# Kernel tuning notes

Hardware: AMD Instinct MI355X
Metric: run time of the kernel (lower is better)

Reference implementation:

```python
import jax, jax.numpy as jnp
import numpy as np

D_MODEL = 1024
N_HEADS = 16
D_HEAD = D_MODEL // N_HEADS
WINDOW = 256
SCALE = D_HEAD ** -0.5


def setup_inputs() -> dict:
    key = jax.random.key(0)
    ks = jax.random.split(key, 5)
    B, S = 2, 2048
    x = jax.random.normal(ks[0], (B, S, D_MODEL), dtype=jnp.float32)
    # weights stored as [d_in, d_out] so forward is x @ W + b
    W_qkv = jax.random.normal(ks[1], (D_MODEL, 3 * D_MODEL), dtype=jnp.float32) * (D_MODEL ** -0.5)
    b_qkv = jnp.zeros((3 * D_MODEL,), dtype=jnp.float32)
    W_out = jax.random.normal(ks[2], (D_MODEL, D_MODEL), dtype=jnp.float32) * (D_MODEL ** -0.5)
    b_out = jnp.zeros((D_MODEL,), dtype=jnp.float32)
    return {"x": x, "W_qkv": W_qkv, "b_qkv": b_qkv, "W_out": W_out, "b_out": b_out}


def _window_mask(S):
    # Faithful to source: keep positions where (i <= j) & (i >= j - WINDOW + 1),
    # i = query index (rows), j = key index (cols). (Anti-causal window, as in repo.)
    idx = jnp.arange(S)
    keep = (idx[:, None] <= idx[None, :]) & (idx[:, None] >= idx[None, :] - WINDOW + 1)
    return keep  # [S, S] bool


def reference(x, W_qkv, b_qkv, W_out, b_out):
    B, S, D = x.shape
    qkv = x @ W_qkv + b_qkv                      # [B,S,3D]
    q, k, v = jnp.split(qkv, 3, axis=-1)
    def heads(t):
        return t.reshape(B, S, N_HEADS, D_HEAD).transpose(0, 2, 1, 3)  # [B,H,S,dh]
    q, k, v = heads(q), heads(k), heads(v)
    attn = jnp.einsum('bhid,bhjd->bhij', q, k) * SCALE  # [B,H,S,S]
    keep = _window_mask(S)
    attn = jnp.where(keep[None, None], attn, -jnp.inf)
    attn = jax.nn.softmax(attn, axis=-1)
    # dropout is identity in eval mode
    out = jnp.einsum('bhij,bhjd->bhid', attn, v)        # [B,H,S,dh]
    out = out.transpose(0, 2, 1, 3).reshape(B, S, D)
    return out @ W_out + b_out
```

## Files before the change

kernel.cpp:

```cpp
#include <hip/hip_runtime.h>

typedef __bf16 bf16x8 __attribute__((ext_vector_type(8)));
typedef float f32x4 __attribute__((ext_vector_type(4)));
typedef unsigned short u16x8 __attribute__((ext_vector_type(8)));
typedef unsigned short u16x4 __attribute__((ext_vector_type(4)));

#define MFMA16(a, b, c) __builtin_amdgcn_mfma_f32_16x16x32_bf16((a), (b), (c), 0, 0, 0)

#define WAIT_VM2  asm volatile("s_waitcnt vmcnt(2)" ::: "memory")
#define WAIT_VM0  asm volatile("s_waitcnt vmcnt(0)" ::: "memory")
#define WAIT_LGKM asm volatile("s_waitcnt lgkmcnt(0)" ::: "memory")
#define BAR       __builtin_amdgcn_s_barrier()

__device__ __forceinline__ unsigned short f2bf(float f) {
  union { float f; unsigned int i; } v; v.f = f;
  unsigned int u = v.i;
  u += 0x7fffu + ((u >> 16) & 1u);
  return (unsigned short)(u >> 16);
}

__device__ __forceinline__ void gload16(const void* g, void* l) {
  __builtin_amdgcn_global_load_lds(
      (const __attribute__((address_space(1))) unsigned int*)g,
      (__attribute__((address_space(3))) unsigned int*)l, 16, 0, 0);
}

__global__ __launch_bounds__(256) void convert_x(const float* __restrict__ X,
                                                 unsigned short* __restrict__ Xb) {
  size_t i = (size_t)(blockIdx.x * 256 + threadIdx.x) * 8;
  f32x4 f0 = *(const f32x4*)(X + i);
  f32x4 f1 = *(const f32x4*)(X + i + 4);
  u16x8 t;
#pragma unroll
  for (int j = 0; j < 4; ++j) { t[j] = f2bf(f0[j]); t[4 + j] = f2bf(f1[j]); }
  *(u16x8*)(Xb + i) = t;
}

__global__ __launch_bounds__(256) void transpose_w(const float* __restrict__ W,
                                                   unsigned short* __restrict__ Wt,
                                                   int N) {
  __shared__ unsigned short t[32][33];
  int tx = threadIdx.x & 31, ty = threadIdx.x >> 5;
  int bx = blockIdx.x;
  int by = blockIdx.y;
#pragma unroll
  for (int j = 0; j < 4; ++j) {
    int r = ty + j * 8;
    t[tx][r] = f2bf(W[(size_t)(by * 32 + r) * N + bx * 32 + tx]);
  }
  __syncthreads();
#pragma unroll
  for (int j = 0; j < 4; ++j) {
    int r = ty + j * 8;
    Wt[(size_t)(bx * 32 + r) * 1024 + by * 32 + tx] = t[r][tx];
  }
}

__global__ __launch_bounds__(512) void gemm_bt(
    const unsigned short* __restrict__ A, const unsigned short* __restrict__ Bt,
    const float* __restrict__ bias,
    unsigned short* __restrict__ O0, unsigned short* __restrict__ O1,
    unsigned short* __restrict__ O2, float* __restrict__ OF, int mode) {
  __shared__ __align__(16) unsigned short As0[128 * 32];
  __shared__ __align__(16) unsigned short Bs0[128 * 32];
  __shared__ __align__(16) unsigned short As1[128 * 32];
  __shared__ __align__(16) unsigned short Bs1[128 * 32];

  const int K = 1024;
  int tid = threadIdx.x;
  int lane = tid & 63, wave = tid >> 6, quad = lane >> 4, l16 = lane & 15;
  int wr = wave >> 2, wc = wave & 3;
  int m0 = blockIdx.x * 128, n0 = blockIdx.y * 128;

  int srow = tid >> 2, su = tid & 3;
  const unsigned short* ag = A + (size_t)(m0 + srow) * K + su * 8;
  const unsigned short* bg = Bt + (size_t)(n0 + srow) * K + su * 8;
  int loff = tid * 16;

  int abase = (wr * 64 + l16) * 64 + quad * 16;
  int bbase = (wc * 32 + l16) * 64 + quad * 16;

  f32x4 acc[4][2];
#pragma unroll
  for (int i = 0; i < 4; ++i)
#pragma unroll
    for (int j = 0; j < 2; ++j) acc[i][j] = f32x4{0.f, 0.f, 0.f, 0.f};

  auto STAGE = [&](int k0, char* Asb, char* Bsb) {
    gload16(ag + k0, Asb + loff);
    gload16(bg + k0, Bsb + loff);
  };
  auto COMPUTE = [&](const char* Asb, const char* Bsb) {
    bf16x8 af[4], bfr[2];
#pragma unroll
    for (int t = 0; t < 4; ++t)
      af[t] = *(const bf16x8*)(Asb + abase + t * 1024);
#pragma unroll
    for (int t = 0; t < 2; ++t)
      bfr[t] = *(const bf16x8*)(Bsb + bbase + t * 1024);
#pragma unroll
    for (int mt = 0; mt < 4; ++mt)
#pragma unroll
      for (int nt = 0; nt < 2; ++nt)
        acc[mt][nt] = MFMA16(af[mt], bfr[nt], acc[mt][nt]);
  };

  STAGE(0, (char*)As0, (char*)Bs0);
  for (int t = 0; t < 30; t += 2) {
    STAGE((t + 1) * 32, (char*)As1, (char*)Bs1);
    WAIT_VM2; BAR;
    COMPUTE((const char*)As0, (const char*)Bs0);
    WAIT_LGKM; BAR;
    STAGE((t + 2) * 32, (char*)As0, (char*)Bs0);
    WAIT_VM2; BAR;
    COMPUTE((const char*)As1, (const char*)Bs1);
    WAIT_LGKM; BAR;
  }
  STAGE(31 * 32, (char*)As1, (char*)Bs1);
  WAIT_VM2; BAR;
  COMPUTE((const char*)As0, (const char*)Bs0);
  WAIT_LGKM; BAR;
  WAIT_VM0; BAR;
  COMPUTE((const char*)As1, (const char*)Bs1);

  if (mode == 0) {
#pragma unroll
    for (int nt = 0; nt < 2; ++nt) {
      int n = n0 + wc * 32 + nt * 16 + l16;
      float bv = bias[n];
      int seg = n >> 10, cc = n & 1023, hh = cc >> 6, d = cc & 63;
#pragma unroll
      for (int mt = 0; mt < 4; ++mt) {
        int mb = m0 + wr * 64 + mt * 16 + quad * 4;
        int b = mb >> 11, s = mb & 2047;
        if (seg == 2) {
          u16x4 pk;
#pragma unroll
          for (int r = 0; r < 4; ++r) pk[r] = f2bf(acc[mt][nt][r] + bv);
          *(u16x4*)&O2[((size_t)((b << 4) + hh) * 64 + d) * 2048 + s] = pk;
        } else {
          unsigned short* O = seg ? O1 : O0;
#pragma unroll
          for (int r = 0; r < 4; ++r)
            O[((size_t)((b << 4) + hh) * 2048 + (s + r)) * 64 + d] = f2bf(acc[mt][nt][r] + bv);
        }
      }
    }
  } else {
#pragma unroll
    for (int nt = 0; nt < 2; ++nt) {
      int n = n0 + wc * 32 + nt * 16 + l16;
      float bv = bias[n];
#pragma unroll
      for (int mt = 0; mt < 4; ++mt) {
        int mb = m0 + wr * 64 + mt * 16 + quad * 4;
#pragma unroll
        for (int r = 0; r < 4; ++r)
          OF[(size_t)(mb + r) * 1024 + n] = acc[mt][nt][r] + bv;
      }
    }
  }
}

__global__ __launch_bounds__(256) void gemm_bt64(
    const unsigned short* __restrict__ A, const unsigned short* __restrict__ Bt,
    const float* __restrict__ bias, float* __restrict__ OF) {
  __shared__ __align__(16) unsigned short As0[64 * 32];
  __shared__ __align__(16) unsigned short Bs0[64 * 32];
  __shared__ __align__(16) unsigned short As1[64 * 32];
  __shared__ __align__(16) unsigned short Bs1[64 * 32];

  const int K = 1024;
  int tid = threadIdx.x;
  int lane = tid & 63, wave = tid >> 6, quad = lane >> 4, l16 = lane & 15;
  int wr = wave >> 1, wc = wave & 1;
  int m0 = blockIdx.x * 64, n0 = blockIdx.y * 64;

  int srow = tid >> 2, su = tid & 3;
  const unsigned short* ag = A + (size_t)(m0 + srow) * K + su * 8;
  const unsigned short* bg = Bt + (size_t)(n0 + srow) * K + su * 8;
  int loff = tid * 16;

  int abase = (wr * 32 + l16) * 64 + quad * 16;
  int bbase = (wc * 32 + l16) * 64 + quad * 16;

  f32x4 acc[2][2];
#pragma unroll
  for (int i = 0; i < 2; ++i)
#pragma unroll
    for (int j = 0; j < 2; ++j) acc[i][j] = f32x4{0.f, 0.f, 0.f, 0.f};

  auto STAGE = [&](int k0, char* Asb, char* Bsb) {
    gload16(ag + k0, Asb + loff);
    gload16(bg + k0, Bsb + loff);
  };
  auto COMPUTE = [&](const char* Asb, const char* Bsb) {
    bf16x8 af[2], bfr[2];
#pragma unroll
    for (int t = 0; t < 2; ++t) {
      af[t]  = *(const bf16x8*)(Asb + abase + t * 1024);
      bfr[t] = *(const bf16x8*)(Bsb + bbase + t * 1024);
    }
#pragma unroll
    for (int mt = 0; mt < 2; ++mt)
#pragma unroll
      for (int nt = 0; nt < 2; ++nt)
        acc[mt][nt] = MFMA16(af[mt], bfr[nt], acc[mt][nt]);
  };

  STAGE(0, (char*)As0, (char*)Bs0);
  for (int t = 0; t < 30; t += 2) {
    STAGE((t + 1) * 32, (char*)As1, (char*)Bs1);
    WAIT_VM2; BAR;
    COMPUTE((const char*)As0, (const char*)Bs0);
    WAIT_LGKM; BAR;
    STAGE((t + 2) * 32, (char*)As0, (char*)Bs0);
    WAIT_VM2; BAR;
    COMPUTE((const char*)As1, (const char*)Bs1);
    WAIT_LGKM; BAR;
  }
  STAGE(31 * 32, (char*)As1, (char*)Bs1);
  WAIT_VM2; BAR;
  COMPUTE((const char*)As0, (const char*)Bs0);
  WAIT_LGKM; BAR;
  WAIT_VM0; BAR;
  COMPUTE((const char*)As1, (const char*)Bs1);

#pragma unroll
  for (int nt = 0; nt < 2; ++nt) {
    int n = n0 + wc * 32 + nt * 16 + l16;
    float bv = bias[n];
#pragma unroll
    for (int mt = 0; mt < 2; ++mt) {
      int mb = m0 + wr * 32 + mt * 16 + quad * 4;
#pragma unroll
      for (int r = 0; r < 4; ++r)
        OF[(size_t)(mb + r) * 1024 + n] = acc[mt][nt][r] + bv;
    }
  }
}

__global__ __launch_bounds__(256) void attn_kernel(
    const unsigned short* __restrict__ Q, const unsigned short* __restrict__ Kq,
    const unsigned short* __restrict__ Vt, unsigned short* __restrict__ AO) {
  __shared__ __align__(16) unsigned short Ps[4][16][40];

  int bid = blockIdx.x;
  int qblk = bid & 31, h = (bid >> 5) & 15, b = bid >> 9;
  int q0 = qblk * 64;
  int tid = threadIdx.x, lane = tid & 63, wave = tid >> 6, quad = lane >> 4, l16 = lane & 15;

  const unsigned short* Qb = Q + (size_t)(((b << 4) + h) * 2048) * 64;
  const unsigned short* Kb = Kq + (size_t)(((b << 4) + h) * 2048) * 64;
  const unsigned short* Vb = Vt + (size_t)(((b << 4) + h) * 64) * 2048;

  int qg = q0 + wave * 16 + l16;
  bf16x8 qf0 = __builtin_bit_cast(bf16x8, *(const u16x8*)&Qb[(size_t)qg * 64 + quad * 8]);
  bf16x8 qf1 = __builtin_bit_cast(bf16x8, *(const u16x8*)&Qb[(size_t)qg * 64 + 32 + quad * 8]);

  float m = -1e30f, l = 0.f;
  f32x4 zero = {0.f, 0.f, 0.f, 0.f};
  f32x4 o[4];
#pragma unroll
  for (int i = 0; i < 4; ++i) o[i] = zero;

  const float SCALE = 0.125f;
  int pstart = (wave >= 2) ? 1 : 0;
  int pend = pstart + 8;

  for (int p = pstart; p <= pend; ++p) {
    int kbase = q0 + p * 32;

    f32x4 sc[2];
    __builtin_amdgcn_s_setprio(1);
#pragma unroll
    for (int t = 0; t < 2; ++t) {
      int krow = kbase + t * 16 + l16;
      krow = krow > 2047 ? 2047 : krow;
      bf16x8 kf0 = __builtin_bit_cast(bf16x8, *(const u16x8*)&Kb[(size_t)krow * 64 + quad * 8]);
      bf16x8 kf1 = __builtin_bit_cast(bf16x8, *(const u16x8*)&Kb[(size_t)krow * 64 + 32 + quad * 8]);
      f32x4 z = zero;
      z = MFMA16(kf0, qf0, z);
      z = MFMA16(kf1, qf1, z);
      sc[t] = z;
    }
    __builtin_amdgcn_s_setprio(0);

    bf16x8 vf[4];
    {
      int vcol = kbase + quad * 8;
      vcol = vcol > 2040 ? 2040 : vcol;
#pragma unroll
      for (int nt = 0; nt < 4; ++nt)
        vf[nt] = __builtin_bit_cast(bf16x8,
            *(const u16x8*)&Vb[(size_t)(nt * 16 + l16) * 2048 + vcol]);
    }

    float sv[2][4];
#pragma unroll
    for (int t = 0; t < 2; ++t)
#pragma unroll
      for (int r = 0; r < 4; ++r) {
        int kg = kbase + t * 16 + quad * 4 + r;
        bool valid = (kg >= qg) && (kg <= qg + 255) && (kg < 2048);
        sv[t][r] = valid ? sc[t][r] * SCALE : -1e30f;
      }

    float vmax = fmaxf(fmaxf(fmaxf(sv[0][0], sv[0][1]), fmaxf(sv[0][2], sv[0][3])),
                       fmaxf(fmaxf(sv[1][0], sv[1][1]), fmaxf(sv[1][2], sv[1][3])));
    vmax = fmaxf(vmax, __shfl_xor(vmax, 16));
    vmax = fmaxf(vmax, __shfl_xor(vmax, 32));
    float mnew = fmaxf(m, vmax);
    float alpha = __expf(m - mnew);
    m = mnew;
    float pe[2][4];
#pragma unroll
    for (int t = 0; t < 2; ++t)
#pragma unroll
      for (int r = 0; r < 4; ++r) {
        float e = __expf(sv[t][r] - mnew);
        pe[t][r] = (sv[t][r] > -5e29f) ? e : 0.f;
      }
    float rs = ((pe[0][0] + pe[0][1]) + (pe[0][2] + pe[0][3])) +
               ((pe[1][0] + pe[1][1]) + (pe[1][2] + pe[1][3]));
    rs += __shfl_xor(rs, 16);
    rs += __shfl_xor(rs, 32);
    l = l * alpha + rs;

    f32x4 av;
#pragma unroll
    for (int r = 0; r < 4; ++r) av[r] = __shfl(alpha, quad * 4 + r);
#pragma unroll
    for (int nt = 0; nt < 4; ++nt) o[nt] *= av;

#pragma unroll
    for (int t = 0; t < 2; ++t) {
      u16x4 pk;
#pragma unroll
      for (int r = 0; r < 4; ++r) pk[r] = f2bf(pe[t][r]);
      *(u16x4*)&Ps[wave][l16][t * 16 + quad * 4] = pk;
    }
    __threadfence_block();
    bf16x8 pf = __builtin_bit_cast(bf16x8, *(const u16x8*)&Ps[wave][l16][quad * 8]);

    __builtin_amdgcn_s_setprio(1);
#pragma unroll
    for (int nt = 0; nt < 4; ++nt)
      o[nt] = MFMA16(pf, vf[nt], o[nt]);
    __builtin_amdgcn_s_setprio(0);
  }

  __threadfence_block();
  float* Lf = (float*)&Ps[wave][0][0];
  Lf[l16] = l;
  __threadfence_block();
  float lr[4];
#pragma unroll
  for (int r = 0; r < 4; ++r) lr[r] = Lf[quad * 4 + r];

  unsigned short* dst = AO + ((size_t)(b * 2048 + q0 + wave * 16) * 1024) + h * 64;
#pragma unroll
  for (int nt = 0; nt < 4; ++nt)
#pragma unroll
    for (int r = 0; r < 4; ++r) {
      int qq = quad * 4 + r;
      dst[(size_t)qq * 1024 + nt * 16 + l16] = f2bf(o[nt][r] / lr[r]);
    }
}

extern "C" void kernel_launch(void* const* d_in, const int* in_sizes, int n_in,
                              void* d_out, int out_size, void* d_ws, size_t ws_size,
                              hipStream_t stream) {
  const float* x = (const float*)d_in[0];
  const float* W_qkv = (const float*)d_in[1];
  const float* b_qkv = (const float*)d_in[2];
  const float* W_out = (const float*)d_in[3];
  const float* b_out = (const float*)d_in[4];
  float* out = (float*)d_out;

  unsigned short* ws = (unsigned short*)d_ws;
  unsigned short* Qw  = ws;
  unsigned short* Kw  = ws + 4194304;
  unsigned short* Vw  = ws + 8388608;
  unsigned short* Wqt = ws + 12582912;
  unsigned short* AO  = ws + 12582912;
  unsigned short* Wot = ws;
  unsigned short* Xb  = (unsigned short*)d_out;

  dim3 blk(256);
  dim3 gblk(512);
  convert_x<<<dim3(2048), blk, 0, stream>>>(x, Xb);
  transpose_w<<<dim3(96, 32), blk, 0, stream>>>(W_qkv, Wqt, 3072);
  gemm_bt<<<dim3(32, 24), gblk, 0, stream>>>(Xb, Wqt, b_qkv, Qw, Kw, Vw, nullptr, 0);
  attn_kernel<<<dim3(1024), blk, 0, stream>>>(Qw, Kw, Vw, AO);
  transpose_w<<<dim3(32, 32), blk, 0, stream>>>(W_out, Wot, 1024);
  gemm_bt64<<<dim3(64, 16), blk, 0, stream>>>(AO, Wot, b_out, out);
}
```

Measured before the change: 175.7 us.

## Merge prep kernels, retile QKV GEMM, skip rescale when max unchanged

Combines the x conversion and both weight transposes into one prep launch and rearranges the workspace so V lives in the output buffer. The QKV GEMM moves from 512-thread 128x128 tiles to 256-thread 128x64 tiles, doubling the grid and adjusting the vmcnt waits. In attention, the output and normaliser rescale is done only when some lane's running max grows, which skips multiplies at the cost of a wave-wide vote and a branch. The aim is to cut launch overhead, raise occupancy and drop redundant softmax work.

After: 181.6 us. 1.03x slower.

```diff
diff --git a/kernel.cpp b/kernel.cpp
--- a/kernel.cpp
+++ b/kernel.cpp
@@ -7,6 +7,7 @@
 
 #define MFMA16(a, b, c) __builtin_amdgcn_mfma_f32_16x16x32_bf16((a), (b), (c), 0, 0, 0)
 
+#define WAIT_VM3  asm volatile("s_waitcnt vmcnt(3)" ::: "memory")
 #define WAIT_VM2  asm volatile("s_waitcnt vmcnt(2)" ::: "memory")
 #define WAIT_VM0  asm volatile("s_waitcnt vmcnt(0)" ::: "memory")
 #define WAIT_LGKM asm volatile("s_waitcnt lgkmcnt(0)" ::: "memory")
@@ -25,24 +26,26 @@
       (__attribute__((address_space(3))) unsigned int*)l, 16, 0, 0);
 }
 
-__global__ __launch_bounds__(256) void convert_x(const float* __restrict__ X,
-                                                 unsigned short* __restrict__ Xb) {
-  size_t i = (size_t)(blockIdx.x * 256 + threadIdx.x) * 8;
-  f32x4 f0 = *(const f32x4*)(X + i);
-  f32x4 f1 = *(const f32x4*)(X + i + 4);
-  u16x8 t;
-#pragma unroll
-  for (int j = 0; j < 4; ++j) { t[j] = f2bf(f0[j]); t[4 + j] = f2bf(f1[j]); }
-  *(u16x8*)(Xb + i) = t;
-}
-
-__global__ __launch_bounds__(256) void transpose_w(const float* __restrict__ W,
-                                                   unsigned short* __restrict__ Wt,
-                                                   int N) {
+__global__ __launch_bounds__(256) void prep(
+    const float* __restrict__ X, const float* __restrict__ Wq,
+    const float* __restrict__ Wo, unsigned short* __restrict__ Xb,
+    unsigned short* __restrict__ Wqt, unsigned short* __restrict__ Wot) {
   __shared__ unsigned short t[32][33];
+  int id = blockIdx.x;
+  if (id < 2048) {
+    size_t i = (size_t)(id * 256 + threadIdx.x) * 8;
+    f32x4 f0 = *(const f32x4*)(X + i);
+    f32x4 f1 = *(const f32x4*)(X + i + 4);
+    u16x8 tt;
+#pragma unroll
+    for (int j = 0; j < 4; ++j) { tt[j] = f2bf(f0[j]); tt[4 + j] = f2bf(f1[j]); }
+    *(u16x8*)(Xb + i) = tt;
+    return;
+  }
+  const float* W; unsigned short* Wt; int N, bx, by;
+  if (id < 5120) { int q = id - 2048; W = Wq; Wt = Wqt; N = 3072; bx = q % 96; by = q / 96; }
+  else           { int q = id - 5120; W = Wo; Wt = Wot; N = 1024; bx = q % 32; by = q / 32; }
   int tx = threadIdx.x & 31, ty = threadIdx.x >> 5;
-  int bx = blockIdx.x;
-  int by = blockIdx.y;
 #pragma unroll
   for (int j = 0; j < 4; ++j) {
     int r = ty + j * 8;
@@ -56,33 +59,139 @@
   }
 }
 
-__global__ __launch_bounds__(512) void gemm_bt(
+__global__ __launch_bounds__(256) void gemm_bt(
     const unsigned short* __restrict__ A, const unsigned short* __restrict__ Bt,
     const float* __restrict__ bias,
     unsigned short* __restrict__ O0, unsigned short* __restrict__ O1,
     unsigned short* __restrict__ O2, float* __restrict__ OF, int mode) {
   __shared__ __align__(16) unsigned short As0[128 * 32];
-  __shared__ __align__(16) unsigned short Bs0[128 * 32];
+  __shared__ __align__(16) unsigned short Bs0[64 * 32];
   __shared__ __align__(16) unsigned short As1[128 * 32];
-  __shared__ __align__(16) unsigned short Bs1[128 * 32];
+  __shared__ __align__(16) unsigned short Bs1[64 * 32];
 
   const int K = 1024;
   int tid = threadIdx.x;
   int lane = tid & 63, wave = tid >> 6, quad = lane >> 4, l16 = lane & 15;
-  int wr = wave >> 2, wc = wave & 3;
-  int m0 = blockIdx.x * 128, n0 = blockIdx.y * 128;
+  int wr = wave >> 1, wc = wave & 1;
+  int m0 = blockIdx.x * 128, n0 = blockIdx.y * 64;
+
+  int srow = tid >> 2, su = tid & 3;
+  const unsigned short* ag0 = A + (size_t)(m0 + srow) * K + su * 8;
+  const unsigned short* ag1 = A + (size_t)(m0 + 64 + srow) * K + su * 8;
+  const unsigned short* bg  = Bt + (size_t)(n0 + srow) * K + su * 8;
+  int aoff0 = tid * 16, aoff1 = (tid + 256) * 16, boff = tid * 16;
+
+  int abase = (wr * 64 + l16) * 64 + quad * 16;
+  int bbase = (wc * 32 + l16) * 64 + quad * 16;
+
+  f32x4 acc[4][2];
+#pragma unroll
+  for (int i = 0; i < 4; ++i)
+#pragma unroll
+    for (int j = 0; j < 2; ++j) acc[i][j] = f32x4{0.f, 0.f, 0.f, 0.f};
+
+  auto STAGE = [&](int k0, char* Asb, char* Bsb) {
+    gload16(ag0 + k0, Asb + aoff0);
+    gload16(ag1 + k0, Asb + aoff1);
+    gload16(bg + k0, Bsb + boff);
+  };
+  auto COMPUTE = [&](const char* Asb, const char* Bsb) {
+    bf16x8 af[4], bfr[2];
+#pragma unroll
+    for (int t = 0; t < 4; ++t)
+      af[t] = *(const bf16x8*)(Asb + abase + t * 1024);
+#pragma unroll
+    for (int t = 0; t < 2; ++t)
+      bfr[t] = *(const bf16x8*)(Bsb + bbase + t * 1024);
+#pragma unroll
+    for (int mt = 0; mt < 4; ++mt)
+#pragma unroll
+      for (int nt = 0; nt < 2; ++nt)
+        acc[mt][nt] = MFMA16(af[mt], bfr[nt], acc[mt][nt]);
+  };
+
+  STAGE(0, (char*)As0, (char*)Bs0);
+  for (int t = 0; t < 30; t += 2) {
+    STAGE((t + 1) * 32, (char*)As1, (char*)Bs1);
+    WAIT_VM3; BAR;
+    COMPUTE((const char*)As0, (const char*)Bs0);
+    WAIT_LGKM; BAR;
+    STAGE((t + 2) * 32, (char*)As0, (char*)Bs0);
+    WAIT_VM3; BAR;
+    COMPUTE((const char*)As1, (const char*)Bs1);
+    WAIT_LGKM; BAR;
+  }
+  STAGE(31 * 32, (char*)As1, (char*)Bs1);
+  WAIT_VM3; BAR;
+  COMPUTE((const char*)As0, (const char*)Bs0);
+  WAIT_LGKM; BAR;
+  WAIT_VM0; BAR;
+  COMPUTE((const char*)As1, (const char*)Bs1);
+
+  if (mode == 0) {
+#pragma unroll
+    for (int nt = 0; nt < 2; ++nt) {
+      int n = n0 + wc * 32 + nt * 16 + l16;
+      float bv = bias[n];
+      int seg = n >> 10, cc = n & 1023, hh = cc >> 6, d = cc & 63;
+#pragma unroll
+      for (int mt = 0; mt < 4; ++mt) {
+        int mb = m0 + wr * 64 + mt * 16 + quad * 4;
+        int b = mb >> 11, s = mb & 2047;
+        if (seg == 2) {
+          u16x4 pk;
+#pragma unroll
+          for (int r = 0; r < 4; ++r) pk[r] = f2bf(acc[mt][nt][r] + bv);
+          *(u16x4*)&O2[((size_t)((b << 4) + hh) * 64 + d) * 2048 + s] = pk;
+        } else {
+          unsigned short* O = seg ? O1 : O0;
+#pragma unroll
+          for (int r = 0; r < 4; ++r)
+            O[((size_t)((b << 4) + hh) * 2048 + (s + r)) * 64 + d] = f2bf(acc[mt][nt][r] + bv);
+        }
+      }
+    }
+  } else {
+#pragma unroll
+    for (int nt = 0; nt < 2; ++nt) {
+      int n = n0 + wc * 32 + nt * 16 + l16;
+      float bv = bias[n];
+#pragma unroll
+      for (int mt = 0; mt < 4; ++mt) {
+        int mb = m0 + wr * 64 + mt * 16 + quad * 4;
+#pragma unroll
+        for (int r = 0; r < 4; ++r)
+          OF[(size_t)(mb + r) * 1024 + n] = acc[mt][nt][r] + bv;
+      }
+    }
+  }
+}
+
+__global__ __launch_bounds__(256) void gemm_bt64(
+    const unsigned short* __restrict__ A, const unsigned short* __restrict__ Bt,
+    const float* __restrict__ bias, float* __restrict__ OF) {
+  __shared__ __align__(16) unsigned short As0[64 * 32];
+  __shared__ __align__(16) unsigned short Bs0[64 * 32];
+  __shared__ __align__(16) unsigned short As1[64 * 32];
+  __shared__ __align__(16) unsigned short Bs1[64 * 32];
+
+  const int K = 1024;
+  int tid = threadIdx.x;
+  int lane = tid & 63, wave = tid >> 6, quad = lane >> 4, l16 = lane & 15;
+  int wr = wave >> 1, wc = wave & 1;
+  int m0 = blockIdx.x * 64, n0 = blockIdx.y * 64;
 
   int srow = tid >> 2, su = tid & 3;
   const unsigned short* ag = A + (size_t)(m0 + srow) * K + su * 8;
   const unsigned short* bg = Bt + (size_t)(n0 + srow) * K + su * 8;
   int loff = tid * 16;
 
-  int abase = (wr * 64 + l16) * 64 + quad * 16;
+  int abase = (wr * 32 + l16) * 64 + quad * 16;
   int bbase = (wc * 32 + l16) * 64 + quad * 16;
 
-  f32x4 acc[4][2];
-#pragma unroll
-  for (int i = 0; i < 4; ++i)
+  f32x4 acc[2][2];
+#pragma unroll
+  for (int i = 0; i < 2; ++i)
 #pragma unroll
     for (int j = 0; j < 2; ++j) acc[i][j] = f32x4{0.f, 0.f, 0.f, 0.f};
 
@@ -91,15 +200,14 @@
     gload16(bg + k0, Bsb + loff);
   };
   auto COMPUTE = [&](const char* Asb, const char* Bsb) {
-    bf16x8 af[4], bfr[2];
-#pragma unroll
-    for (int t = 0; t < 4; ++t)
-      af[t] = *(const bf16x8*)(Asb + abase + t * 1024);
-#pragma unroll
-    for (int t = 0; t < 2; ++t)
+    bf16x8 af[2], bfr[2];
+#pragma unroll
+    for (int t = 0; t < 2; ++t) {
+      af[t]  = *(const bf16x8*)(Asb + abase + t * 1024);
       bfr[t] = *(const bf16x8*)(Bsb + bbase + t * 1024);
-#pragma unroll
-    for (int mt = 0; mt < 4; ++mt)
+    }
+#pragma unroll
+    for (int mt = 0; mt < 2; ++mt)
 #pragma unroll
       for (int nt = 0; nt < 2; ++nt)
         acc[mt][nt] = MFMA16(af[mt], bfr[nt], acc[mt][nt]);
@@ -123,109 +231,6 @@
   WAIT_VM0; BAR;
   COMPUTE((const char*)As1, (const char*)Bs1);
 
-  if (mode == 0) {
-#pragma unroll
-    for (int nt = 0; nt < 2; ++nt) {
-      int n = n0 + wc * 32 + nt * 16 + l16;
-      float bv = bias[n];
-      int seg = n >> 10, cc = n & 1023, hh = cc >> 6, d = cc & 63;
-#pragma unroll
-      for (int mt = 0; mt < 4; ++mt) {
-        int mb = m0 + wr * 64 + mt * 16 + quad * 4;
-        int b = mb >> 11, s = mb & 2047;
-        if (seg == 2) {
-          u16x4 pk;
-#pragma unroll
-          for (int r = 0; r < 4; ++r) pk[r] = f2bf(acc[mt][nt][r] + bv);
-          *(u16x4*)&O2[((size_t)((b << 4) + hh) * 64 + d) * 2048 + s] = pk;
-        } else {
-          unsigned short* O = seg ? O1 : O0;
-#pragma unroll
-          for (int r = 0; r < 4; ++r)
-            O[((size_t)((b << 4) + hh) * 2048 + (s + r)) * 64 + d] = f2bf(acc[mt][nt][r] + bv);
-        }
-      }
-    }
-  } else {
-#pragma unroll
-    for (int nt = 0; nt < 2; ++nt) {
-      int n = n0 + wc * 32 + nt * 16 + l16;
-      float bv = bias[n];
-#pragma unroll
-      for (int mt = 0; mt < 4; ++mt) {
-        int mb = m0 + wr * 64 + mt * 16 + quad * 4;
-#pragma unroll
-        for (int r = 0; r < 4; ++r)
-          OF[(size_t)(mb + r) * 1024 + n] = acc[mt][nt][r] + bv;
-      }
-    }
-  }
-}
-
-__global__ __launch_bounds__(256) void gemm_bt64(
-    const unsigned short* __restrict__ A, const unsigned short* __restrict__ Bt,
-    const float* __restrict__ bias, float* __restrict__ OF) {
-  __shared__ __align__(16) unsigned short As0[64 * 32];
-  __shared__ __align__(16) unsigned short Bs0[64 * 32];
-  __shared__ __align__(16) unsigned short As1[64 * 32];
-  __shared__ __align__(16) unsigned short Bs1[64 * 32];
-
-  const int K = 1024;
-  int tid = threadIdx.x;
-  int lane = tid & 63, wave = tid >> 6, quad = lane >> 4, l16 = lane & 15;
-  int wr = wave >> 1, wc = wave & 1;
-  int m0 = blockIdx.x * 64, n0 = blockIdx.y * 64;
-
-  int srow = tid >> 2, su = tid & 3;
-  const unsigned short* ag = A + (size_t)(m0 + srow) * K + su * 8;
-  const unsigned short* bg = Bt + (size_t)(n0 + srow) * K + su * 8;
-  int loff = tid * 16;
-
-  int abase = (wr * 32 + l16) * 64 + quad * 16;
-  int bbase = (wc * 32 + l16) * 64 + quad * 16;
-
-  f32x4 acc[2][2];
-#pragma unroll
-  for (int i = 0; i < 2; ++i)
-#pragma unroll
-    for (int j = 0; j < 2; ++j) acc[i][j] = f32x4{0.f, 0.f, 0.f, 0.f};
-
-  auto STAGE = [&](int k0, char* Asb, char* Bsb) {
-    gload16(ag + k0, Asb + loff);
-    gload16(bg + k0, Bsb + loff);
-  };
-  auto COMPUTE = [&](const char* Asb, const char* Bsb) {
-    bf16x8 af[2], bfr[2];
-#pragma unroll
-    for (int t = 0; t < 2; ++t) {
-      af[t]  = *(const bf16x8*)(Asb + abase + t * 1024);
-      bfr[t] = *(const bf16x8*)(Bsb + bbase + t * 1024);
-    }
-#pragma unroll
-    for (int mt = 0; mt < 2; ++mt)
-#pragma unroll
-      for (int nt = 0; nt < 2; ++nt)
-        acc[mt][nt] = MFMA16(af[mt], bfr[nt], acc[mt][nt]);
-  };
-
-  STAGE(0, (char*)As0, (char*)Bs0);
-  for (int t = 0; t < 30; t += 2) {
-    STAGE((t + 1) * 32, (char*)As1, (char*)Bs1);
-    WAIT_VM2; BAR;
-    COMPUTE((const char*)As0, (const char*)Bs0);
-    WAIT_LGKM; BAR;
-    STAGE((t + 2) * 32, (char*)As0, (char*)Bs0);
-    WAIT_VM2; BAR;
-    COMPUTE((const char*)As1, (const char*)Bs1);
-    WAIT_LGKM; BAR;
-  }
-  STAGE(31 * 32, (char*)As1, (char*)Bs1);
-  WAIT_VM2; BAR;
-  COMPUTE((const char*)As0, (const char*)Bs0);
-  WAIT_LGKM; BAR;
-  WAIT_VM0; BAR;
-  COMPUTE((const char*)As1, (const char*)Bs1);
-
 #pragma unroll
   for (int nt = 0; nt < 2; ++nt) {
     int n = n0 + wc * 32 + nt * 16 + l16;
@@ -311,8 +316,6 @@
     vmax = fmaxf(vmax, __shfl_xor(vmax, 16));
     vmax = fmaxf(vmax, __shfl_xor(vmax, 32));
     float mnew = fmaxf(m, vmax);
-    float alpha = __expf(m - mnew);
-    m = mnew;
     float pe[2][4];
 #pragma unroll
     for (int t = 0; t < 2; ++t)
@@ -325,13 +328,19 @@
                ((pe[1][0] + pe[1][1]) + (pe[1][2] + pe[1][3]));
     rs += __shfl_xor(rs, 16);
     rs += __shfl_xor(rs, 32);
-    l = l * alpha + rs;
-
-    f32x4 av;
-#pragma unroll
-    for (int r = 0; r < 4; ++r) av[r] = __shfl(alpha, quad * 4 + r);
-#pragma unroll
-    for (int nt = 0; nt < 4; ++nt) o[nt] *= av;
+
+    if (__any(vmax > m)) {
+      float alpha = __expf(m - mnew);
+      m = mnew;
+      l = l * alpha + rs;
+      f32x4 av;
+#pragma unroll
+      for (int r = 0; r < 4; ++r) av[r] = __shfl(alpha, quad * 4 + r);
+#pragma unroll
+      for (int nt = 0; nt < 4; ++nt) o[nt] *= av;
+    } else {
+      l += rs;
+    }
 
 #pragma unroll
     for (int t = 0; t < 2; ++t) {
@@ -381,18 +390,15 @@
   unsigned short* ws = (unsigned short*)d_ws;
   unsigned short* Qw  = ws;
   unsigned short* Kw  = ws + 4194304;
-  unsigned short* Vw  = ws + 8388608;
-  unsigned short* Wqt = ws + 12582912;
+  unsigned short* Wqt = ws + 8388608;
+  unsigned short* Wot = ws + 11534336;
   unsigned short* AO  = ws + 12582912;
-  unsigned short* Wot = ws;
   unsigned short* Xb  = (unsigned short*)d_out;
+  unsigned short* Vw  = (unsigned short*)d_out + 4194304;
 
   dim3 blk(256);
-  dim3 gblk(512);
-  convert_x<<<dim3(2048), blk, 0, stream>>>(x, Xb);
-  transpose_w<<<dim3(96, 32), blk, 0, stream>>>(W_qkv, Wqt, 3072);
-  gemm_bt<<<dim3(32, 24), gblk, 0, stream>>>(Xb, Wqt, b_qkv, Qw, Kw, Vw, nullptr, 0);
+  prep<<<dim3(6144), blk, 0, stream>>>(x, W_qkv, W_out, Xb, Wqt, Wot);
+  gemm_bt<<<dim3(32, 48), blk, 0, stream>>>(Xb, Wqt, b_qkv, Qw, Kw, Vw, nullptr, 0);
   attn_kernel<<<dim3(1024), blk, 0, stream>>>(Qw, Kw, Vw, AO);
-  transpose_w<<<dim3(32, 32), blk, 0, stream>>>(W_out, Wot, 1024);
   gemm_bt64<<<dim3(64, 16), blk, 0, stream>>>(AO, Wot, b_out, out);
 }
```
